# Optimization experiments

Measured on AMD Instinct MI355X. Metric: run time of the kernel, lower is better.

The kernel has to match this reference:

```python
import jax, jax.numpy as jnp
import numpy as np

MAX_DISP = 24   # maxDisp = 192/8
K = 3           # box-filter kernel size
PAD = 1         # conv padding


def _cost_volume(inputs):
    # inputs: [B, 2c, H, W]; first half is input1, second half is input2
    b, c2, h, w = inputs.shape
    c = c2 // 2
    x1 = inputs[:, :c]
    x2 = inputs[:, c:]
    # pad input2 on the left by MAX_DISP (matches Fun.pad(..., (max_disp,0,0,0)))
    x2p = jnp.pad(x2, ((0, 0), (0, 0), (0, 0), (MAX_DISP, 0)))
    # original loop: d = MAX_DISP .. 0, slice [d:d+w]; output channel i uses
    # d = MAX_DISP - i, i.e. input2 shifted right by i pixels.
    slices = [
        jnp.einsum('bchw,bchw->bhw', x1,
                   x2p[:, :, :, MAX_DISP - i:MAX_DISP - i + w])
        for i in range(MAX_DISP + 1)
    ]
    corr = jnp.stack(slices, axis=1)  # [B, D+1, H, W]
    # per-channel (depthwise) conv with an all-ones KxK kernel == original
    # single-channel conv2d applied to each disparity slice
    ones = jnp.ones((MAX_DISP + 1, 1, K, K), dtype=inputs.dtype)
    out = jax.lax.conv_general_dilated(
        corr, ones,
        window_strides=(1, 1),
        padding=((PAD, PAD), (PAD, PAD)),
        feature_group_count=MAX_DISP + 1,
        dimension_numbers=('NCHW', 'OIHW', 'NCHW'))
    return out  # [B, MAX_DISP+1, H, W]


def setup_inputs() -> dict:
    key = jax.random.key(0)
    inputs = jax.random.normal(key, (16, 512, 64, 192), dtype=jnp.float32)
    return {"inputs": inputs}


def reference(inputs):
    return _cost_volume(inputs)
```

## Files before the change

### kernel.cpp

```cpp
#include <hip/hip_runtime.h>

constexpr int Bq = 16;
constexpr int Cc = 256;
constexpr int Hh = 64;
constexpr int Ww = 192;
constexpr int Dd = 25;
constexpr int HW = Hh * Ww;
constexpr int BSTRIDE = 2 * Cc * HW;
constexpr int CPR = 4;
constexpr int NR = Cc / CPR;
constexpr int ROWP = 24 + Ww;

__global__ __launch_bounds__(192) void corr_kernel(const float* __restrict__ in,
                                                   float* __restrict__ corr) {
  const int t   = threadIdx.x;
  const int hg  = blockIdx.x;
  const int b   = blockIdx.y;
  const int row = t / 96;
  const int u   = t % 96;
  const int w0  = 2 * u;
  const int h   = hg * 2 + row;

  __shared__ float x2s[2][CPR][ROWP];

  {
    const int r2  = t / (CPR * 24);
    const int rem = t % (CPR * 24);
    x2s[r2][rem / 24][rem % 24] = 0.0f;
  }

  const float* x1p = in + (size_t)b * BSTRIDE + (size_t)h * Ww + w0;
  const float* x2p = x1p + (size_t)Cc * HW;

  float2 acc[Dd];
#pragma unroll
  for (int d = 0; d < Dd; ++d) acc[d] = make_float2(0.0f, 0.0f);

  float2 px1[CPR], px2[CPR];
#pragma unroll
  for (int c = 0; c < CPR; ++c) {
    px1[c] = *(const float2*)(x1p + c * HW);
    px2[c] = *(const float2*)(x2p + c * HW);
  }

  for (int rnd = 0; rnd < NR; ++rnd) {
    __syncthreads();
    float2 cx1[CPR];
#pragma unroll
    for (int c = 0; c < CPR; ++c) {
      cx1[c] = px1[c];
      *(float2*)&x2s[row][c][24 + w0] = px2[c];
    }
    __syncthreads();

    if (rnd + 1 < NR) {
      const float* p1 = x1p + (size_t)(rnd + 1) * CPR * HW;
      const float* p2 = p1 + (size_t)Cc * HW;
#pragma unroll
      for (int c = 0; c < CPR; ++c) {
        px1[c] = *(const float2*)(p1 + c * HW);
        px2[c] = *(const float2*)(p2 + c * HW);
      }
    }

#pragma unroll
    for (int c = 0; c < CPR; ++c) {
      float win[26];
#pragma unroll
      for (int k = 0; k < 13; ++k) {
        const float2 v = *(const float2*)&x2s[row][c][w0 + 2 * k];
        win[2 * k]     = v.x;
        win[2 * k + 1] = v.y;
      }
      const float a0 = cx1[c].x, a1 = cx1[c].y;
#pragma unroll
      for (int d = 0; d < Dd; ++d) {
        acc[d].x = fmaf(a0, win[24 - d], acc[d].x);
        acc[d].y = fmaf(a1, win[25 - d], acc[d].y);
      }
    }
  }

  float* cp = corr + ((size_t)b * Dd * Hh + h) * Ww + w0;
#pragma unroll
  for (int d = 0; d < Dd; ++d)
    *(float2*)(cp + (size_t)d * HW) = acc[d];
}

__global__ __launch_bounds__(192) void box_kernel(const float* __restrict__ corr,
                                                  float* __restrict__ out) {
  const int w  = threadIdx.x;
  const int h  = blockIdx.x;
  const int bd = blockIdx.y;
  const float* base = corr + ((size_t)bd * Hh + h) * Ww;

  float s = 0.0f;
#pragma unroll
  for (int dh = -1; dh <= 1; ++dh) {
    const int hh = h + dh;
    if (hh < 0 || hh >= Hh) continue;
    const float* r = base + dh * Ww;
    s += r[w];
    if (w > 0)      s += r[w - 1];
    if (w < Ww - 1) s += r[w + 1];
  }
  out[((size_t)bd * Hh + h) * Ww + w] = s;
}

extern "C" void kernel_launch(void* const* d_in, const int* in_sizes, int n_in,
                              void* d_out, int out_size, void* d_ws, size_t ws_size,
                              hipStream_t stream) {
  const float* in = (const float*)d_in[0];
  float* out  = (float*)d_out;
  float* corr = (float*)d_ws;

  dim3 g1(Hh / 2, Bq);
  corr_kernel<<<g1, 192, 0, stream>>>(in, corr);

  dim3 g2(Hh, Bq * Dd);
  box_kernel<<<g2, Ww, 0, stream>>>(corr, out);
}
```

Measured before the change: 545.9 us.

## Split channel reduction across grid z and sum partials in box filter

The correlation kernel now splits the 256-channel reduction into four slices along a third grid dimension, so it launches four times as many blocks. Each slice writes its own partial cost volume to workspace. The box kernel sums the four partials while applying the vertical 3-tap filter, then does the horizontal 3-tap through shared memory. This targets low occupancy, since the old grid had only 512 blocks on a many-CU GPU. The cost is four times the intermediate write and read traffic plus a larger workspace.

After: 591.6 us. 8.4% more time.

```diff
diff --git a/kernel.cpp b/kernel.cpp
--- a/kernel.cpp
+++ b/kernel.cpp
@@ -8,14 +8,18 @@
 constexpr int HW = Hh * Ww;
 constexpr int BSTRIDE = 2 * Cc * HW;
 constexpr int CPR = 4;
-constexpr int NR = Cc / CPR;
+constexpr int NS = 4;
+constexpr int CS = Cc / NS;
+constexpr int NR = CS / CPR;
 constexpr int ROWP = 24 + Ww;
+constexpr size_t PLANE = (size_t)Bq * Dd * Hh * Ww;
 
 __global__ __launch_bounds__(192) void corr_kernel(const float* __restrict__ in,
-                                                   float* __restrict__ corr) {
+                                                   float* __restrict__ part) {
   const int t   = threadIdx.x;
   const int hg  = blockIdx.x;
   const int b   = blockIdx.y;
+  const int s   = blockIdx.z;
   const int row = t / 96;
   const int u   = t % 96;
   const int w0  = 2 * u;
@@ -29,7 +33,8 @@
     x2s[r2][rem / 24][rem % 24] = 0.0f;
   }
 
-  const float* x1p = in + (size_t)b * BSTRIDE + (size_t)h * Ww + w0;
+  const float* x1p = in + (size_t)b * BSTRIDE + (size_t)(s * CS) * HW
+                        + (size_t)h * Ww + w0;
   const float* x2p = x1p + (size_t)Cc * HW;
 
   float2 acc[Dd];
@@ -81,30 +86,35 @@
     }
   }
 
-  float* cp = corr + ((size_t)b * Dd * Hh + h) * Ww + w0;
+  float* cp = part + s * PLANE + ((size_t)b * Dd * Hh + h) * Ww + w0;
 #pragma unroll
   for (int d = 0; d < Dd; ++d)
     *(float2*)(cp + (size_t)d * HW) = acc[d];
 }
 
-__global__ __launch_bounds__(192) void box_kernel(const float* __restrict__ corr,
+__global__ __launch_bounds__(192) void box_kernel(const float* __restrict__ part,
                                                   float* __restrict__ out) {
   const int w  = threadIdx.x;
   const int h  = blockIdx.x;
   const int bd = blockIdx.y;
-  const float* base = corr + ((size_t)bd * Hh + h) * Ww;
 
-  float s = 0.0f;
+  __shared__ float v[Ww + 2];
+  if (w == 0)  v[0] = 0.0f;
+  if (w == 1)  v[Ww + 1] = 0.0f;
+
+  float sum = 0.0f;
 #pragma unroll
-  for (int dh = -1; dh <= 1; ++dh) {
-    const int hh = h + dh;
-    if (hh < 0 || hh >= Hh) continue;
-    const float* r = base + dh * Ww;
-    s += r[w];
-    if (w > 0)      s += r[w - 1];
-    if (w < Ww - 1) s += r[w + 1];
+  for (int si = 0; si < NS; ++si) {
+    const float* base = part + si * PLANE + ((size_t)bd * Hh + h) * Ww;
+#pragma unroll
+    for (int dh = -1; dh <= 1; ++dh) {
+      const int hh = h + dh;
+      if (hh >= 0 && hh < Hh) sum += base[(size_t)dh * Ww + w];
+    }
   }
-  out[((size_t)bd * Hh + h) * Ww + w] = s;
+  v[w + 1] = sum;
+  __syncthreads();
+  out[((size_t)bd * Hh + h) * Ww + w] = v[w] + v[w + 1] + v[w + 2];
 }
 
 extern "C" void kernel_launch(void* const* d_in, const int* in_sizes, int n_in,
@@ -112,11 +122,11 @@
                               hipStream_t stream) {
   const float* in = (const float*)d_in[0];
   float* out  = (float*)d_out;
-  float* corr = (float*)d_ws;
+  float* part = (float*)d_ws;
 
-  dim3 g1(Hh / 2, Bq);
-  corr_kernel<<<g1, 192, 0, stream>>>(in, corr);
+  dim3 g1(Hh / 2, Bq, NS);
+  corr_kernel<<<g1, 192, 0, stream>>>(in, part);
 
   dim3 g2(Hh, Bq * Dd);
-  box_kernel<<<g2, Ww, 0, stream>>>(corr, out);
+  box_kernel<<<g2, Ww, 0, stream>>>(part, out);
 }
```

## Double-buffer shared x2 tiles, widen channel chunk, separable box filter

Applied to the files above, without the earlier changes.

The correlation kernel now processes 8 channels per round and double-buffers the shared input2 rows, computing on the previous round's buffer while the current one is written. This drops one barrier per round and halves the number of rounds. The box kernel sums vertically first, then does the horizontal 3-tap through shared memory, which reduces global loads. In exchange it uses more registers (px1, px2, cx1, a1 arrays) and more shared memory, which may lower occupancy.

After: 549.6 us. About the same (+0.7%).

```diff
diff --git a/kernel.cpp b/kernel.cpp
--- a/kernel.cpp
+++ b/kernel.cpp
@@ -7,7 +7,7 @@
 constexpr int Dd = 25;
 constexpr int HW = Hh * Ww;
 constexpr int BSTRIDE = 2 * Cc * HW;
-constexpr int CPR = 4;
+constexpr int CPR = 8;
 constexpr int NR = Cc / CPR;
 constexpr int ROWP = 24 + Ww;
 
@@ -21,12 +21,16 @@
   const int w0  = 2 * u;
   const int h   = hg * 2 + row;
 
-  __shared__ float x2s[2][CPR][ROWP];
+  __shared__ float x2s[2][2][CPR][ROWP];
 
-  {
-    const int r2  = t / (CPR * 24);
-    const int rem = t % (CPR * 24);
-    x2s[r2][rem / 24][rem % 24] = 0.0f;
+#pragma unroll
+  for (int i = 0; i < 4; ++i) {
+    const int idx  = i * 192 + t;
+    const int buf  = idx / (2 * CPR * 24);
+    const int rem  = idx % (2 * CPR * 24);
+    const int rr   = rem / (CPR * 24);
+    const int rem2 = rem % (CPR * 24);
+    x2s[buf][rr][rem2 / 24][rem2 % 24] = 0.0f;
   }
 
   const float* x1p = in + (size_t)b * BSTRIDE + (size_t)h * Ww + w0;
@@ -36,47 +40,72 @@
 #pragma unroll
   for (int d = 0; d < Dd; ++d) acc[d] = make_float2(0.0f, 0.0f);
 
-  float2 px1[CPR], px2[CPR];
+  float2 px1[CPR], px2[CPR], cx1[CPR];
 #pragma unroll
   for (int c = 0; c < CPR; ++c) {
-    px1[c] = *(const float2*)(x1p + c * HW);
-    px2[c] = *(const float2*)(x2p + c * HW);
+    px1[c] = *(const float2*)(x1p + (size_t)c * HW);
+    px2[c] = *(const float2*)(x2p + (size_t)c * HW);
   }
 
-  for (int rnd = 0; rnd < NR; ++rnd) {
+  for (int r = 0; r < NR; ++r) {
     __syncthreads();
-    float2 cx1[CPR];
+
+    float2 a1[CPR];
 #pragma unroll
     for (int c = 0; c < CPR; ++c) {
+      *(float2*)&x2s[r & 1][row][c][24 + w0] = px2[c];
+      a1[c]  = cx1[c];
       cx1[c] = px1[c];
-      *(float2*)&x2s[row][c][24 + w0] = px2[c];
     }
-    __syncthreads();
 
-    if (rnd + 1 < NR) {
-      const float* p1 = x1p + (size_t)(rnd + 1) * CPR * HW;
+    if (r + 1 < NR) {
+      const float* p1 = x1p + (size_t)(r + 1) * CPR * HW;
       const float* p2 = p1 + (size_t)Cc * HW;
 #pragma unroll
       for (int c = 0; c < CPR; ++c) {
-        px1[c] = *(const float2*)(p1 + c * HW);
-        px2[c] = *(const float2*)(p2 + c * HW);
+        px1[c] = *(const float2*)(p1 + (size_t)c * HW);
+        px2[c] = *(const float2*)(p2 + (size_t)c * HW);
       }
     }
 
+    if (r > 0) {
+      const int rb = (r - 1) & 1;
+#pragma unroll
+      for (int c = 0; c < CPR; ++c) {
+        float win[26];
+#pragma unroll
+        for (int k = 0; k < 13; ++k) {
+          const float2 v = *(const float2*)&x2s[rb][row][c][w0 + 2 * k];
+          win[2 * k]     = v.x;
+          win[2 * k + 1] = v.y;
+        }
+        const float a0 = a1[c].x, b0 = a1[c].y;
+#pragma unroll
+        for (int d = 0; d < Dd; ++d) {
+          acc[d].x = fmaf(a0, win[24 - d], acc[d].x);
+          acc[d].y = fmaf(b0, win[25 - d], acc[d].y);
+        }
+      }
+    }
+  }
+
+  __syncthreads();
+  {
+    const int rb = (NR - 1) & 1;
 #pragma unroll
     for (int c = 0; c < CPR; ++c) {
       float win[26];
 #pragma unroll
       for (int k = 0; k < 13; ++k) {
-        const float2 v = *(const float2*)&x2s[row][c][w0 + 2 * k];
+        const float2 v = *(const float2*)&x2s[rb][row][c][w0 + 2 * k];
         win[2 * k]     = v.x;
         win[2 * k + 1] = v.y;
       }
-      const float a0 = cx1[c].x, a1 = cx1[c].y;
+      const float a0 = cx1[c].x, b0 = cx1[c].y;
 #pragma unroll
       for (int d = 0; d < Dd; ++d) {
         acc[d].x = fmaf(a0, win[24 - d], acc[d].x);
-        acc[d].y = fmaf(a1, win[25 - d], acc[d].y);
+        acc[d].y = fmaf(b0, win[25 - d], acc[d].y);
       }
     }
   }
@@ -92,19 +121,21 @@
   const int w  = threadIdx.x;
   const int h  = blockIdx.x;
   const int bd = blockIdx.y;
+
+  __shared__ float v[Ww + 2];
+  if (w == 0)  v[0] = 0.0f;
+  if (w == 1)  v[Ww + 1] = 0.0f;
+
   const float* base = corr + ((size_t)bd * Hh + h) * Ww;
-
-  float s = 0.0f;
+  float sum = 0.0f;
 #pragma unroll
   for (int dh = -1; dh <= 1; ++dh) {
     const int hh = h + dh;
-    if (hh < 0 || hh >= Hh) continue;
-    const float* r = base + dh * Ww;
-    s += r[w];
-    if (w > 0)      s += r[w - 1];
-    if (w < Ww - 1) s += r[w + 1];
+    if (hh >= 0 && hh < Hh) sum += base[(size_t)dh * Ww + w];
   }
-  out[((size_t)bd * Hh + h) * Ww + w] = s;
+  v[w + 1] = sum;
+  __syncthreads();
+  out[((size_t)bd * Hh + h) * Ww + w] = v[w] + v[w + 1] + v[w + 2];
 }
 
 extern "C" void kernel_launch(void* const* d_in, const int* in_sizes, int n_in,
```
